# Performance work log

Hardware: AMD Instinct MI355X
Metric: run time of the kernel (lower is better)

The kernel has to match this reference:

```python
import jax, jax.numpy as jnp
import numpy as np

MAXDISP = 21  # default maxDisp from __init__


def _make_kernel():
    # convweights[i,0,:,0:2] = 1/6 ; convweights[i,0,:,i+2] = -1/3 ; bias[i] = i+1
    w = np.zeros((MAXDISP, 1, 3, MAXDISP + 2), dtype=np.float32)
    for i in range(MAXDISP):
        w[i, 0, :, 0:2] = 1.0 / 6.0
        w[i, 0, :, i + 2] = -1.0 / 3.0
    b = np.arange(1, MAXDISP + 1, dtype=np.float32)
    return jnp.asarray(w), jnp.asarray(b)


def _compute_mask(disp, w, b):
    # ReplicationPad2d((left=0, right=maxDisp+1, top=1, bottom=1))
    pad = jnp.pad(disp, ((0, 0), (0, 0), (1, 1), (0, MAXDISP + 1)), mode='edge')
    # conv2d, VALID: output spatial size == input spatial size
    out = jax.lax.conv_general_dilated(
        pad, w, window_strides=(1, 1), padding='VALID',
        dimension_numbers=('NCHW', 'OIHW', 'NCHW'))
    out = jnp.abs(out + b[None, :, None, None])          # [B, maxDisp, H, W]
    mask = jnp.min(out, axis=1, keepdims=True)           # channel-min -> [B,1,H,W]
    return jnp.clip(mask, 0.0, 1.0)


def _forward(dispmap, bsline):
    w, b = _make_kernel()
    maskl = _compute_mask(dispmap, w, b)
    # 'r' direction: flip along width, compute, flip back
    maskr = jnp.flip(_compute_mask(jnp.flip(dispmap, axis=3), w, b), axis=3)
    bs = bsline[:, None, None, None]
    zero = jnp.zeros_like(dispmap)
    # bsline < 0 -> left mask; bsline > 0 -> right mask; else zeros
    return jnp.where(bs < 0, maskl, jnp.where(bs > 0, maskr, zero))


def setup_inputs() -> dict:
    key = jax.random.key(0)
    k1, k2 = jax.random.split(key)
    # disparity-like values in [0, 1)
    dispmap = jax.random.uniform(k1, (8, 1, 384, 1280), dtype=jnp.float32)
    bsline = jax.random.normal(k2, (8,), dtype=jnp.float32)
    return {"dispmap": dispmap, "bsline": bsline}


def reference(dispmap, bsline):
    return _forward(dispmap, bsline)
```

## Files before the change

### kernel.cpp

```cpp
#include <hip/hip_runtime.h>

#define W  1280
#define H  384
#define ND 21
#define BT 320


template <int DIR>
__device__ __forceinline__ void compute4(const float* __restrict__ Cs,
                                         float* __restrict__ orow, int t) {
    float V[28];
    const float4* p = (const float4*)(Cs + ((DIR > 0) ? 4 * t : 4 * t - 24));
    #pragma unroll
    for (int m = 0; m < 7; m++) {
        float4 f = p[m];
        V[4 * m + 0] = f.x; V[4 * m + 1] = f.y;
        V[4 * m + 2] = f.z; V[4 * m + 3] = f.w;
    }
    float4 o;
    float* op = &o.x;
    #pragma unroll
    for (int j = 0; j < 4; j++) {
        float c0 = (DIR > 0) ? V[j]     : V[24 + j];
        float c1 = (DIR > 0) ? V[j + 1] : V[23 + j];
        float base = (c0 + c1) * (1.0f / 6.0f);
        float m = 1e30f;
        #pragma unroll
        for (int i = 0; i < ND; i++) {
            float ck = (DIR > 0) ? V[j + 2 + i] : V[22 + j - i];
            float v = fabsf(base + (float)(i + 1) - ck * (1.0f / 3.0f));
            m = fminf(m, v);
        }
        op[j] = fminf(m, 1.0f);
    }
    ((float4*)orow)[t] = o;
}

__global__ __launch_bounds__(BT) void occl_kernel(const float* __restrict__ disp,
                                                  const float* __restrict__ bsl,
                                                  float* __restrict__ out) {
    int g = blockIdx.x;
    int nb = gridDim.x;
    int id = (nb & 7) ? g : ((g & 7) * (nb >> 3) + (g >> 3));
    const int row = id % H;
    const int batch = id / H;
    const float bs = bsl[batch];
    float* __restrict__ orow = out + (size_t)(batch * H + row) * W;
    const int t = threadIdx.x;

    if (bs == 0.0f) {
        float4 z = {0.0f, 0.0f, 0.0f, 0.0f};
        ((float4*)orow)[t] = z;
        return;
    }

    __shared__ float Cbuf[W + 48];
    float* Cs = Cbuf + 24;

    const float* __restrict__ dbase = disp + (size_t)batch * H * W;
    const float* __restrict__ r0 = dbase + (size_t)max(row - 1, 0) * W;
    const float* __restrict__ r1 = dbase + (size_t)row * W;
    const float* __restrict__ r2 = dbase + (size_t)min(row + 1, H - 1) * W;

    float4 a = ((const float4*)r0)[t];
    float4 b = ((const float4*)r1)[t];
    float4 c = ((const float4*)r2)[t];
    float4 s;
    s.x = a.x + b.x + c.x;
    s.y = a.y + b.y + c.y;
    s.z = a.z + b.z + c.z;
    s.w = a.w + b.w + c.w;
    ((float4*)Cs)[t] = s;

    if (t < 24) {
        Cs[t - 24] = r0[0] + r1[0] + r2[0];
    } else if (t >= 32 && t < 56) {
        Cs[W + (t - 32)] = r0[W - 1] + r1[W - 1] + r2[W - 1];
    }
    __syncthreads();

    if (bs < 0.0f) compute4<1>(Cs, orow, t);
    else           compute4<-1>(Cs, orow, t);
}

extern "C" void kernel_launch(void* const* d_in, const int* in_sizes, int n_in,
                              void* d_out, int out_size, void* d_ws, size_t ws_size,
                              hipStream_t stream) {
    const float* disp = (const float*)d_in[0];
    const float* bsl  = (const float*)d_in[1];
    float* out        = (float*)d_out;
    const int n_batch = in_sizes[1];

    occl_kernel<<<dim3(n_batch * H), BT, 0, stream>>>(disp, bsl, out);
}
```

Baseline: 75.37 us.

## Process four rows per block with rolling row registers and double-buffered shared memory

Each block now computes four consecutive output rows, keeping the three input rows in registers and rotating them so each new row needs only one extra global load. Column sums go into a double-buffered shared array, so one barrier per row is enough. The inner loop is also rewritten algebraically: per-column terms k - c/3 are precomputed once and shared across the four outputs, which cuts per-element arithmetic. The grid shrinks fourfold, which lowers parallelism and adds more serial work per block.

```diff
diff --git a/kernel.cpp b/kernel.cpp
--- a/kernel.cpp
+++ b/kernel.cpp
@@ -4,83 +4,106 @@
 #define H  384
 #define ND 21
 #define BT 320
-
+#define R  4
 
 template <int DIR>
-__device__ __forceinline__ void compute4(const float* __restrict__ Cs,
-                                         float* __restrict__ orow, int t) {
+__device__ __forceinline__ void compute_row(const float* __restrict__ Cs,
+                                            float* __restrict__ orow, int t) {
     float V[28];
     const float4* p = (const float4*)(Cs + ((DIR > 0) ? 4 * t : 4 * t - 24));
     #pragma unroll
     for (int m = 0; m < 7; m++) {
         float4 f = p[m];
-        V[4 * m + 0] = f.x; V[4 * m + 1] = f.y;
-        V[4 * m + 2] = f.z; V[4 * m + 3] = f.w;
+        V[4*m+0] = f.x; V[4*m+1] = f.y; V[4*m+2] = f.z; V[4*m+3] = f.w;
     }
-    float4 o;
-    float* op = &o.x;
+    float Q[24];
+    #pragma unroll
+    for (int m = 0; m < 24; m++) {
+        float k = (DIR > 0) ? (float)(m + 1) : (float)(21 - m);
+        Q[m] = k - V[m + 2] * (1.0f / 3.0f);
+    }
+    float4 o; float* op = &o.x;
     #pragma unroll
     for (int j = 0; j < 4; j++) {
-        float c0 = (DIR > 0) ? V[j]     : V[24 + j];
-        float c1 = (DIR > 0) ? V[j + 1] : V[23 + j];
-        float base = (c0 + c1) * (1.0f / 6.0f);
-        float m = 1e30f;
+        float base = (DIR > 0) ? (V[j] + V[j+1]) * (1.0f / 6.0f)
+                               : (V[24+j] + V[23+j]) * (1.0f / 6.0f);
+        float B = (DIR > 0) ? (base - (float)j) : (base + (float)j);
+        float m0 = 1e30f;
         #pragma unroll
-        for (int i = 0; i < ND; i++) {
-            float ck = (DIR > 0) ? V[j + 2 + i] : V[22 + j - i];
-            float v = fabsf(base + (float)(i + 1) - ck * (1.0f / 3.0f));
-            m = fminf(m, v);
-        }
-        op[j] = fminf(m, 1.0f);
+        for (int i = 0; i < ND; i++)
+            m0 = fminf(m0, fabsf(B + Q[j + i]));
+        op[j] = fminf(m0, 1.0f);
     }
     ((float4*)orow)[t] = o;
+}
+
+template <int DIR>
+__device__ __forceinline__ void run_rows(const float* __restrict__ dbase,
+                                         float* __restrict__ outb,
+                                         float (*Cbuf)[W + 48],
+                                         int rs, int t) {
+    const bool lp = (t < 24);
+    const bool rp = (t >= 32 && t < 56);
+    const int  ecol = lp ? 0 : (W - 1);
+
+    int r0 = max(rs - 1, 0);
+    float4 a = ((const float4*)(dbase + (size_t)r0       * W))[t];
+    float4 b = ((const float4*)(dbase + (size_t)rs       * W))[t];
+    float4 c = ((const float4*)(dbase + (size_t)(rs + 1) * W))[t];
+    float4 d = {0, 0, 0, 0};
+    float ea = 0, eb = 0, ec = 0, ed = 0;
+    if (lp || rp) {
+        ea = dbase[(size_t)r0       * W + ecol];
+        eb = dbase[(size_t)rs       * W + ecol];
+        ec = dbase[(size_t)(rs + 1) * W + ecol];
+    }
+
+    #pragma unroll
+    for (int r = 0; r < R; r++) {
+        float* Cs = Cbuf[r & 1] + 24;
+        float4 s;
+        s.x = a.x + b.x + c.x; s.y = a.y + b.y + c.y;
+        s.z = a.z + b.z + c.z; s.w = a.w + b.w + c.w;
+        ((float4*)Cs)[t] = s;
+        if (lp)      Cs[t - 24]      = ea + eb + ec;
+        else if (rp) Cs[W + (t - 32)] = ea + eb + ec;
+
+        if (r + 1 < R) {
+            int nr = min(rs + r + 2, H - 1);
+            d = ((const float4*)(dbase + (size_t)nr * W))[t];
+            if (lp || rp) ed = dbase[(size_t)nr * W + ecol];
+        }
+        __syncthreads();
+        compute_row<DIR>(Cs, outb + (size_t)r * W, t);
+        a = b; b = c; c = d;
+        ea = eb; eb = ec; ec = ed;
+    }
 }
 
 __global__ __launch_bounds__(BT) void occl_kernel(const float* __restrict__ disp,
                                                   const float* __restrict__ bsl,
                                                   float* __restrict__ out) {
-    int g = blockIdx.x;
-    int nb = gridDim.x;
+    int g = blockIdx.x, nb = gridDim.x;
     int id = (nb & 7) ? g : ((g & 7) * (nb >> 3) + (g >> 3));
-    const int row = id % H;
-    const int batch = id / H;
+    const int RB = H / R;
+    const int batch = id / RB;
+    const int rs = (id % RB) * R;
     const float bs = bsl[batch];
-    float* __restrict__ orow = out + (size_t)(batch * H + row) * W;
     const int t = threadIdx.x;
+    float* outb = out + ((size_t)batch * H + rs) * W;
 
     if (bs == 0.0f) {
-        float4 z = {0.0f, 0.0f, 0.0f, 0.0f};
-        ((float4*)orow)[t] = z;
+        float4 z = {0, 0, 0, 0};
+        #pragma unroll
+        for (int r = 0; r < R; r++) ((float4*)(outb + (size_t)r * W))[t] = z;
         return;
     }
 
-    __shared__ float Cbuf[W + 48];
-    float* Cs = Cbuf + 24;
+    __shared__ float Cbuf[2][W + 48];
+    const float* dbase = disp + (size_t)batch * H * W;
 
-    const float* __restrict__ dbase = disp + (size_t)batch * H * W;
-    const float* __restrict__ r0 = dbase + (size_t)max(row - 1, 0) * W;
-    const float* __restrict__ r1 = dbase + (size_t)row * W;
-    const float* __restrict__ r2 = dbase + (size_t)min(row + 1, H - 1) * W;
-
-    float4 a = ((const float4*)r0)[t];
-    float4 b = ((const float4*)r1)[t];
-    float4 c = ((const float4*)r2)[t];
-    float4 s;
-    s.x = a.x + b.x + c.x;
-    s.y = a.y + b.y + c.y;
-    s.z = a.z + b.z + c.z;
-    s.w = a.w + b.w + c.w;
-    ((float4*)Cs)[t] = s;
-
-    if (t < 24) {
-        Cs[t - 24] = r0[0] + r1[0] + r2[0];
-    } else if (t >= 32 && t < 56) {
-        Cs[W + (t - 32)] = r0[W - 1] + r1[W - 1] + r2[W - 1];
-    }
-    __syncthreads();
-
-    if (bs < 0.0f) compute4<1>(Cs, orow, t);
-    else           compute4<-1>(Cs, orow, t);
+    if (bs < 0.0f) run_rows<1>(dbase, outb, Cbuf, rs, t);
+    else           run_rows<-1>(dbase, outb, Cbuf, rs, t);
 }
 
 extern "C" void kernel_launch(void* const* d_in, const int* in_sizes, int n_in,
@@ -91,5 +114,5 @@
     float* out        = (float*)d_out;
     const int n_batch = in_sizes[1];
 
-    occl_kernel<<<dim3(n_batch * H), BT, 0, stream>>>(disp, bsl, out);
+    occl_kernel<<<dim3(n_batch * (H / R)), BT, 0, stream>>>(disp, bsl, out);
 }
```

Measured after the change: 75.15 us. No clear change (-0.3%).
